# Kernel optimization log

Hardware: AMD Instinct MI355X
Metric: run time of the kernel (lower is better)

## Reference

```python
import jax, jax.numpy as jnp
import numpy as np

EPS = 1e-5

def _offset_conv(x, w, b):
    # 3x3 conv, padding=1, producing 2*K*K offset channels (standard DeformConv2D v1)
    out = jax.lax.conv_general_dilated(x, w, (1, 1), ((1, 1), (1, 1)),
                                       dimension_numbers=('NCHW', 'OIHW', 'NCHW'))
    return out + b[None, :, None, None]

def _bilinear_gather(x, py, px):
    # x: [B,C,H,W]; py,px: [B,K2,H,W] float sample coords -> [B,C,K2,H,W]
    B, C, H, W = x.shape
    py = jnp.clip(py, 0.0, H - 1.0)
    px = jnp.clip(px, 0.0, W - 1.0)
    y0 = jnp.floor(py)
    x0 = jnp.floor(px)
    wy = py - y0
    wx = px - x0
    y0i = y0.astype(jnp.int32)
    x0i = x0.astype(jnp.int32)
    y1i = jnp.minimum(y0i + 1, H - 1)
    x1i = jnp.minimum(x0i + 1, W - 1)
    xf = x.reshape(B, C, H * W)
    K2, Ho, Wo = py.shape[1], py.shape[2], py.shape[3]
    def gather(yy, xx):
        idx = (yy * W + xx).reshape(B, 1, -1)  # broadcast over C
        return jnp.take_along_axis(xf, idx, axis=2).reshape(B, C, K2, Ho, Wo)
    v00 = gather(y0i, x0i)
    v01 = gather(y0i, x1i)
    v10 = gather(y1i, x0i)
    v11 = gather(y1i, x1i)
    wy = wy[:, None]
    wx = wx[:, None]
    return (v00 * (1 - wy) * (1 - wx) + v01 * (1 - wy) * wx
            + v10 * wy * (1 - wx) + v11 * wy * wx)

def _deform_dw(x, w_off, b_off, w_dw, k):
    # depthwise deformable conv, kernel k, padding k//2 (same spatial size)
    B, C, H, W = x.shape
    K2 = k * k
    off = _offset_conv(x, w_off, b_off)      # [B, 2*K2, H, W]
    dy, dx = off[:, :K2], off[:, K2:]
    r = (k - 1) // 2
    pn = jnp.arange(-r, r + 1, dtype=x.dtype)
    pn_y = jnp.repeat(pn, k)[None, :, None, None]  # [1,K2,1,1]
    pn_x = jnp.tile(pn, k)[None, :, None, None]
    gy = jnp.arange(H, dtype=x.dtype)[None, None, :, None]
    gx = jnp.arange(W, dtype=x.dtype)[None, None, None, :]
    py = gy + pn_y + dy
    px = gx + pn_x + dx
    samp = _bilinear_gather(x, py, px)        # [B,C,K2,H,W]
    return jnp.einsum('bckhw,ck->bchw', samp, w_dw.reshape(C, K2))

def _bn_relu(x, g, b, m, v):
    inv = g / jnp.sqrt(v + EPS)
    return jax.nn.relu(x * inv[None, :, None, None] + (b - m * inv)[None, :, None, None])

def setup_inputs() -> dict:
    key = jax.random.key(0)
    B, C, H, W, O = 4, 96, 64, 64, 192
    ks = jax.random.split(key, 32)
    d = {'x': jax.random.normal(ks[0], (B, C, H, W), jnp.float32)}
    i = 1
    for k in (3, 5, 7):
        K2 = k * k
        d[f'w_off{k}'] = 0.01 * jax.random.normal(ks[i], (2 * K2, C, 3, 3), jnp.float32); i += 1
        d[f'b_off{k}'] = jnp.zeros((2 * K2,), jnp.float32)
        d[f'w_dw{k}'] = jax.random.normal(ks[i], (C, k, k), jnp.float32) / k; i += 1
        d[f'g{k}'] = jnp.ones((C,), jnp.float32)
        d[f'be{k}'] = jnp.zeros((C,), jnp.float32)
        d[f'm{k}'] = 0.1 * jax.random.normal(ks[i], (C,), jnp.float32); i += 1
        d[f'v{k}'] = jax.random.uniform(ks[i], (C,), jnp.float32, 0.5, 1.5); i += 1
    d['w_pw'] = jax.random.normal(ks[i], (O, 3 * C), jnp.float32) / np.sqrt(3 * C).astype(np.float32); i += 1
    d['gp'] = jnp.ones((O,), jnp.float32)
    d['bp'] = jnp.zeros((O,), jnp.float32)
    d['mp'] = 0.1 * jax.random.normal(ks[i], (O,), jnp.float32); i += 1
    d['vp'] = jax.random.uniform(ks[i], (O,), jnp.float32, 0.5, 1.5)
    return d

def reference(x, w_off3, b_off3, w_dw3, g3, be3, m3, v3,
              w_off5, b_off5, w_dw5, g5, be5, m5, v5,
              w_off7, b_off7, w_dw7, g7, be7, m7, v7,
              w_pw, gp, bp, mp, vp):
    x1 = _bn_relu(_deform_dw(x, w_off3, b_off3, w_dw3, 3), g3, be3, m3, v3)
    x2 = _bn_relu(_deform_dw(x, w_off5, b_off5, w_dw5, 5), g5, be5, m5, v5)
    x3 = _bn_relu(_deform_dw(x, w_off7, b_off7, w_dw7, 7), g7, be7, m7, v7)
    xc = jnp.concatenate([x1, x2, x3], axis=1)  # [B, 3C, H, W]
    out = jnp.einsum('bchw,oc->bohw', xc, w_pw)  # 1x1 conv
    return _bn_relu(out, gp, bp, mp, vp)
```

## Files before the change

kernel.cpp:

```cpp
#include <hip/hip_runtime.h>
#include <hip/hip_fp16.h>
#include <math.h>

typedef unsigned short u16;
typedef _Float16 f16x8 __attribute__((ext_vector_type(8)));
typedef float f32x4 __attribute__((ext_vector_type(4)));

#define HWp 4096
#define Cc 96
#define Bb 4
#define Oo 192
#define C3 288

#define OFF_WDWT  0
#define OFF_BCAT  14112
#define OFF_SBR   14304
#define OFF_HBR   14592
#define OFF_SPW   14880
#define OFF_HPW   15072
#define FP32_END  15264
#define BF_XTPAD  0
#define BF_WOF    1672704
#define BF_WPW    1838592

__device__ __forceinline__ u16 f2h(float f) { return __half_as_ushort(__float2half(f)); }
__device__ __forceinline__ unsigned h2u(__half2 h) { union { __half2 h; unsigned u; } t; t.h = h; return t.u; }
__device__ __forceinline__ __half2 u2h(unsigned u) { union { __half2 h; unsigned u; } t; t.u = u; return t.h; }

#define PREP_N (165888 + 55296 + 14112 + 192 + 288 + 288 + 192 + 192 + 24960)
#define PREP_BLK ((PREP_N + 255) / 256)

__global__ __launch_bounds__(256) void prep_kernel(
    const float* __restrict__ x,
    const float* __restrict__ w3, const float* __restrict__ b3, const float* __restrict__ dw3,
    const float* __restrict__ g3, const float* __restrict__ be3, const float* __restrict__ m3, const float* __restrict__ v3,
    const float* __restrict__ w5, const float* __restrict__ b5, const float* __restrict__ dw5,
    const float* __restrict__ g5, const float* __restrict__ be5, const float* __restrict__ m5, const float* __restrict__ v5,
    const float* __restrict__ w7, const float* __restrict__ b7, const float* __restrict__ dw7,
    const float* __restrict__ g7, const float* __restrict__ be7, const float* __restrict__ m7, const float* __restrict__ v7,
    const float* __restrict__ wpw,
    const float* __restrict__ gp, const float* __restrict__ bp, const float* __restrict__ mp, const float* __restrict__ vp,
    float* __restrict__ ws)
{
    __shared__ u16 sT[64 * 104];
    u16* bf = (u16*)(ws + FP32_END);
    const int tid = threadIdx.x;

    if (blockIdx.x < 256) {
        const int b = blockIdx.x >> 6, h = blockIdx.x & 63;
        const float* xb = x + (((size_t)b * Cc) << 12) + (h << 6);
#pragma unroll
        for (int it = 0; it < 24; ++it) {
            int j = tid + it * 256;
            int c = j >> 6, p = j & 63;
            sT[p * 104 + c] = f2h(xb[((size_t)c << 12) + p]);
        }
        __syncthreads();
        u16* dst = bf + BF_XTPAD + ((size_t)(b * 66 + h + 1) * 66 + 1) * 96;
#pragma unroll
        for (int it = 0; it < 6; ++it) {
            int j = tid + it * 256;
            int pos = j / 24, c4 = j % 24;
            const u16* s = &sT[pos * 104 + c4 * 4];
            *(uint2*)(dst + pos * 96 + c4 * 4) = make_uint2(
                (unsigned)s[0] | ((unsigned)s[1] << 16),
                (unsigned)s[2] | ((unsigned)s[3] << 16));
        }
        return;
    }

    int i = (blockIdx.x - 256) * 256 + tid;
    if (i < 165888) {
        int f = i / 13824, r = i % 13824;
        int s = r >> 9, l = r & 511;
        int lane = l >> 3, j = l & 7;
        int o = f * 16 + (lane & 15);
        int k = s * 32 + (lane >> 4) * 8 + j;
        int tap = k / 96, c = k % 96;
        float v = 0.f;
        if (o < 18)       v = w3[o * 864 + c * 9 + tap];
        else if (o < 68)  v = w5[(o - 18) * 864 + c * 9 + tap];
        else if (o < 166) v = w7[(o - 68) * 864 + c * 9 + tap];
        bf[BF_WOF + i] = f2h(v);
        return;
    }
    int j = i - 165888;
    if (j < 55296) {
        int f = j / 4608, r = j % 4608;
        int s = r >> 9, l = r & 511;
        int lane = l >> 3, jj = l & 7;
        int o = f * 16 + (lane & 15);
        int k = s * 32 + (lane >> 4) * 8 + jj;
        bf[BF_WPW + j] = f2h(wpw[o * C3 + k]);
        return;
    }
    j -= 55296;
    if (j < 14112) {
        int ksel = j / 4704, rem = j % 4704;
        int t = rem / 96, c = rem % 96;
        int K2 = (ksel == 0) ? 9 : (ksel == 1) ? 25 : 49;
        const float* dw = (ksel == 0) ? dw3 : (ksel == 1) ? dw5 : dw7;
        ws[OFF_WDWT + j] = (t < K2) ? dw[c * K2 + t] : 0.f;
        return;
    }
    j -= 14112;
    if (j < 192) {
        float v = 0.f;
        if (j < 18)       v = b3[j];
        else if (j < 68)  v = b5[j - 18];
        else if (j < 166) v = b7[j - 68];
        ws[OFF_BCAT + j] = v;
        return;
    }
    j -= 192;
    if (j < C3) {
        int ks = j / Cc, c = j % Cc;
        const float* g = (ks == 0) ? g3 : (ks == 1) ? g5 : g7;
        const float* v = (ks == 0) ? v3 : (ks == 1) ? v5 : v7;
        ws[OFF_SBR + j] = g[c] / sqrtf(v[c] + 1e-5f);
        return;
    }
    j -= C3;
    if (j < C3) {
        int ks = j / Cc, c = j % Cc;
        const float* g = (ks == 0) ? g3 : (ks == 1) ? g5 : g7;
        const float* v = (ks == 0) ? v3 : (ks == 1) ? v5 : v7;
        const float* be = (ks == 0) ? be3 : (ks == 1) ? be5 : be7;
        const float* m = (ks == 0) ? m3 : (ks == 1) ? m5 : m7;
        float inv = g[c] / sqrtf(v[c] + 1e-5f);
        ws[OFF_HBR + j] = be[c] - m[c] * inv;
        return;
    }
    j -= C3;
    if (j < Oo) { ws[OFF_SPW + j] = gp[j] / sqrtf(vp[j] + 1e-5f); return; }
    j -= Oo;
    if (j < Oo) {
        float inv = gp[j] / sqrtf(vp[j] + 1e-5f);
        ws[OFF_HPW + j] = bp[j] - mp[j] * inv;
        return;
    }
    j -= Oo;
    if (j < 24960) {
        int c4 = j % 24, rem = j / 24;
        int cell = rem % 260, bb = rem / 260;
        int row, col;
        if (cell < 66)       { row = 0;  col = cell; }
        else if (cell < 132) { row = 65; col = cell - 66; }
        else if (cell < 196) { row = cell - 132 + 1; col = 0; }
        else                 { row = cell - 196 + 1; col = 65; }
        u16* dst = bf + BF_XTPAD + ((size_t)(bb * 66 + row) * 66 + col) * 96 + c4 * 4;
        *(uint2*)dst = make_uint2(0u, 0u);
        return;
    }
}

__global__ __launch_bounds__(256, 4) void mega_kernel(
    const float* __restrict__ ws, float* __restrict__ out)
{
    __shared__ __align__(16) unsigned char shA[15936];
    __shared__ float regB[3072];
    __shared__ float sP1[1728];
    u16* sX = (u16*)shA;
    uint2* sWab = (uint2*)shA;
    unsigned* sPk = (unsigned*)(shA + 10624);
    float* soff = regB;
    u16* ytile = (u16*)regB;

    const u16* bf = (const u16*)(ws + FP32_END);
    const u16* xp = bf + BF_XTPAD;
    const int tid = threadIdx.x;
    const int lane = tid & 63, wid = tid >> 6;
    const int lane15 = lane & 15, quad = lane >> 4;

    const int bx = blockIdx.x;
    const int xcd = bx & 7;
    const int b = xcd >> 1;
    const int tile = ((bx >> 3) << 1) + (xcd & 1);
    const int p0 = tile * 16;
    const int h = p0 >> 6;
    const int w0 = p0 & 63;

    {
        const u16* src = xp + ((size_t)(b * 66 + h) * 66 + w0) * 96;
        for (int j = tid; j < 1296; j += 256) {
            int r = j / 432;
            int rem = j % 432;
            int col = rem / 24, c4 = rem % 24;
            uint2 v = *(const uint2*)(src + ((size_t)(r * 66 + col)) * 96 + c4 * 4);
            *(uint2*)(&sX[(r * 18 + col) * 104 + c4 * 4]) = v;
        }
    }
    __syncthreads();

    {
        const u16* wof = bf + BF_WOF;
        f32x4 acc[3];
#pragma unroll
        for (int ff = 0; ff < 3; ++ff) acc[ff] = (f32x4){0.f, 0.f, 0.f, 0.f};
#pragma unroll
        for (int tap = 0; tap < 9; ++tap) {
            const int ky2 = tap / 3, kx2 = tap % 3;
            const u16* brow = &sX[(ky2 * 18 + kx2 + lane15) * 104 + quad * 8];
#pragma unroll
            for (int cc = 0; cc < 3; ++cc) {
                f16x8 bb = *(const f16x8*)(brow + cc * 32);
                const int s = tap * 3 + cc;
#pragma unroll
                for (int ff = 0; ff < 3; ++ff) {
                    const int f = wid * 3 + ff;
                    f16x8 a = *(const f16x8*)(wof + ((size_t)(f * 27 + s) * 64 + lane) * 8);
                    acc[ff] = __builtin_amdgcn_mfma_f32_16x16x32_f16(a, bb, acc[ff], 0, 0, 0);
                }
            }
        }
        const float* bcat = ws + OFF_BCAT;
#pragma unroll
        for (int ff = 0; ff < 3; ++ff) {
#pragma unroll
            for (int r = 0; r < 4; ++r) {
                int co = (wid * 3 + ff) * 16 + quad * 4 + r;
                soff[co * 16 + lane15] = acc[ff][r] + bcat[co];
            }
        }
    }
    __syncthreads();

    for (int i = tid; i < 1328; i += 256) {
        int gt = i >> 4, q = i & 15;
        int K, K2, R, tb, t;
        if (gt < 9)       { K = 3; K2 = 9;  R = 1; tb = 0;  t = gt; }
        else if (gt < 34) { K = 5; K2 = 25; R = 2; tb = 18; t = gt - 9; }
        else              { K = 7; K2 = 49; R = 3; tb = 68; t = gt - 34; }
        int ky = t / K - R, kx = t % K - R;
        float dy = soff[(tb + t) * 16 + q];
        float dx = soff[(tb + K2 + t) * 16 + q];
        float py = fminf(fmaxf((float)(h + ky) + dy, 0.f), 63.f);
        float px = fminf(fmaxf((float)(w0 + q + kx) + dx, 0.f), 63.f);
        float fy = floorf(py), fx = floorf(px);
        int y0 = (int)fy, x0 = (int)fx;
        float wy = py - fy, wx = px - fx;
        float w11 = wy * wx;
        float w10 = wy - w11;
        float w01 = wx - w11;
        float w00 = 1.f - wy - wx + w11;
        sWab[i] = make_uint2(h2u(__floats2half2_rn(w00, w01)),
                             h2u(__floats2half2_rn(w10, w11)));
        sPk[i] = (unsigned)((y0 + 1) * 66 + (x0 + 1)) * 192u;
    }
    __syncthreads();

#define TAP8(ACC, GT, Q, XCB, WDP) { \
    const uint2 wab = sWab[((GT) << 4) + (Q)]; \
    const unsigned o00 = sPk[((GT) << 4) + (Q)]; \
    const __half2 wAh = u2h(wab.x), wBh = u2h(wab.y); \
    const __half2 w00b = __low2half2(wAh), w01b = __high2half2(wAh); \
    const __half2 w10b = __low2half2(wBh), w11b = __high2half2(wBh); \
    const char* pb = (XCB) + o00; \
    const uint4 u00 = *(const uint4*)(pb); \
    const uint4 u01 = *(const uint4*)(pb + 192); \
    const uint4 u10 = *(const uint4*)(pb + 12672); \
    const uint4 u11 = *(const uint4*)(pb + 12864); \
    const float4 wda = *(const float4*)(WDP); \
    const float4 wdb = *(const float4*)((WDP) + 4); \
    const unsigned a00[4] = {u00.x, u00.y, u00.z, u00.w}; \
    const unsigned a01[4] = {u01.x, u01.y, u01.z, u01.w}; \
    const unsigned a10[4] = {u10.x, u10.y, u10.z, u10.w}; \
    const unsigned a11[4] = {u11.x, u11.y, u11.z, u11.w}; \
    const float wd8[8] = {wda.x, wda.y, wda.z, wda.w, wdb.x, wdb.y, wdb.z, wdb.w}; \
    _Pragma("unroll") \
    for (int d = 0; d < 4; ++d) { \
        __half2 v = __hmul2(w00b, u2h(a00[d])); \
        v = __hfma2(w01b, u2h(a01[d]), v); \
        v = __hfma2(w10b, u2h(a10[d]), v); \
        v = __hfma2(w11b, u2h(a11[d]), v); \
        ACC[2 * d]     = fmaf(wd8[2 * d],     __low2float(v),  ACC[2 * d]); \
        ACC[2 * d + 1] = fmaf(wd8[2 * d + 1], __high2float(v), ACC[2 * d + 1]); \
    } }

#define BN_STORE(ACC, CB, Q) { \
    const float4 sa = *(const float4*)(ws + OFF_SBR + (CB)); \
    const float4 sb = *(const float4*)(ws + OFF_SBR + (CB) + 4); \
    const float4 ha = *(const float4*)(ws + OFF_HBR + (CB)); \
    const float4 hb = *(const float4*)(ws + OFF_HBR + (CB) + 4); \
    const float ss8[8] = {sa.x, sa.y, sa.z, sa.w, sb.x, sb.y, sb.z, sb.w}; \
    const float hh8[8] = {ha.x, ha.y, ha.z, ha.w, hb.x, hb.y, hb.z, hb.w}; \
    unsigned rr[4]; \
    _Pragma("unroll") \
    for (int d = 0; d < 4; ++d) { \
        float lo = fmaxf(fmaf(ACC[2 * d],     ss8[2 * d],     hh8[2 * d]),     0.f); \
        float hi = fmaxf(fmaf(ACC[2 * d + 1], ss8[2 * d + 1], hh8[2 * d + 1]), 0.f); \
        rr[d] = h2u(__floats2half2_rn(lo, hi)); \
    } \
    *(uint4*)(ytile + (Q) * 296 + (CB)) = make_uint4(rr[0], rr[1], rr[2], rr[3]); }

    const u16* xh = xp + (size_t)b * 66 * 66 * 96;

    if (tid < 192) {
        const int c8 = tid % 12;
        const int q  = tid / 12;
        const int c = c8 * 8;
        const char* xcb = (const char*)xh + c * 2;

        {
            float acc[8] = {0.f, 0.f, 0.f, 0.f, 0.f, 0.f, 0.f, 0.f};
            const float* wdT = ws + OFF_WDWT + c;
            for (int gt = 0; gt < 9; ++gt)
                TAP8(acc, gt, q, xcb, wdT + gt * 96);
            BN_STORE(acc, c, q);
        }
        {
            float acc[8] = {0.f, 0.f, 0.f, 0.f, 0.f, 0.f, 0.f, 0.f};
            const float* wdT = ws + OFF_WDWT + 9408 + c;
            for (int gt = 34; gt < 83; ++gt)
                TAP8(acc, gt, q, xcb, wdT + (gt - 34) * 96);
            BN_STORE(acc, 192 + c, q);
        }
        __syncthreads();
        {
            float acc[8] = {0.f, 0.f, 0.f, 0.f, 0.f, 0.f, 0.f, 0.f};
            const float* wdT = ws + OFF_WDWT + 4704 + c;
            for (int gt = 9; gt < 17; ++gt)
                TAP8(acc, gt, q, xcb, wdT + (gt - 9) * 96);
#pragma unroll
            for (int jj = 0; jj < 8; ++jj) acc[jj] += sP1[tid * 9 + jj];
            BN_STORE(acc, 96 + c, q);
        }
    } else {
        const int s = tid - 192;
#pragma unroll 1
        for (int k = 0; k < 3; ++k) {
            const int slot = 3 * s + k;
            const int q2 = slot / 12;
            const int c2 = (slot % 12) * 8;
            const char* xcb2 = (const char*)xh + c2 * 2;
            const float* wdT = ws + OFF_WDWT + 4704 + c2;
            float acc[8] = {0.f, 0.f, 0.f, 0.f, 0.f, 0.f, 0.f, 0.f};
            for (int gt = 17; gt < 34; ++gt)
                TAP8(acc, gt, q2, xcb2, wdT + (gt - 9) * 96);
#pragma unroll
            for (int jj = 0; jj < 8; ++jj) sP1[slot * 9 + jj] = acc[jj];
        }
        __syncthreads();
    }
    __syncthreads();

    {
        const u16* wpw = bf + BF_WPW;
        f32x4 acc[3];
#pragma unroll
        for (int ff = 0; ff < 3; ++ff) acc[ff] = (f32x4){0.f, 0.f, 0.f, 0.f};
        const u16* brow = &ytile[lane15 * 296 + quad * 8];
#pragma unroll
        for (int s = 0; s < 9; ++s) {
            f16x8 bb = *(const f16x8*)(brow + s * 32);
#pragma unroll
            for (int ff = 0; ff < 3; ++ff) {
                const int f = wid * 3 + ff;
                f16x8 a = *(const f16x8*)(wpw + ((size_t)(f * 9 + s) * 64 + lane) * 8);
                acc[ff] = __builtin_amdgcn_mfma_f32_16x16x32_f16(a, bb, acc[ff], 0, 0, 0);
            }
        }
        const float* spw = ws + OFF_SPW;
        const float* hpw = ws + OFF_HPW;
        const int p = p0 + lane15;
#pragma unroll
        for (int ff = 0; ff < 3; ++ff) {
#pragma unroll
            for (int r = 0; r < 4; ++r) {
                int o = (wid * 3 + ff) * 16 + quad * 4 + r;
                out[(((size_t)(b * Oo + o)) << 12) + p] =
                    fmaxf(fmaf(acc[ff][r], spw[o], hpw[o]), 0.f);
            }
        }
    }
}

extern "C" void kernel_launch(void* const* d_in, const int* in_sizes, int n_in,
                              void* d_out, int out_size, void* d_ws, size_t ws_size,
                              hipStream_t stream)
{
    const float* x     = (const float*)d_in[0];
    const float* w3    = (const float*)d_in[1];
    const float* b3    = (const float*)d_in[2];
    const float* dw3   = (const float*)d_in[3];
    const float* g3    = (const float*)d_in[4];
    const float* be3   = (const float*)d_in[5];
    const float* m3    = (const float*)d_in[6];
    const float* v3    = (const float*)d_in[7];
    const float* w5    = (const float*)d_in[8];
    const float* b5    = (const float*)d_in[9];
    const float* dw5   = (const float*)d_in[10];
    const float* g5    = (const float*)d_in[11];
    const float* be5   = (const float*)d_in[12];
    const float* m5    = (const float*)d_in[13];
    const float* v5    = (const float*)d_in[14];
    const float* w7    = (const float*)d_in[15];
    const float* b7    = (const float*)d_in[16];
    const float* dw7   = (const float*)d_in[17];
    const float* g7    = (const float*)d_in[18];
    const float* be7   = (const float*)d_in[19];
    const float* m7    = (const float*)d_in[20];
    const float* v7    = (const float*)d_in[21];
    const float* wpw   = (const float*)d_in[22];
    const float* gp    = (const float*)d_in[23];
    const float* bp    = (const float*)d_in[24];
    const float* mp    = (const float*)d_in[25];
    const float* vp    = (const float*)d_in[26];

    float* ws = (float*)d_ws;
    float* out = (float*)d_out;

    {
        prep_kernel<<<256 + PREP_BLK, 256, 0, stream>>>(
            x,
            w3, b3, dw3, g3, be3, m3, v3,
            w5, b5, dw5, g5, be5, m5, v5,
            w7, b7, dw7, g7, be7, m7, v7,
            wpw, gp, bp, mp, vp, ws);
    }
    {
        mega_kernel<<<1024, 256, 0, stream>>>(ws, out);
    }
}
```

Baseline: 178.7 us.

## Stage input rows in a shared-memory ring buffer for bilinear gathers

Bilinear samples for the three deformable depthwise convs now come from a 3-row LDS ring buffer holding a 27-pixel-wide window of the padded input. The buffer is refilled row by row as the kernel-row loop advances, and samples that fall outside the window fall back to global loads. Taps are reorganized by kernel row so all three kernel sizes accumulate together. This replaces the old split of 192 compute threads plus 64 helper threads and drops the sP1 partial-sum buffer. Per-sample metadata shrinks to packed half (wy,wx) and a 16-bit coordinate, with the four bilinear weights recomputed in half precision. The cost is extra barriers per row, divergent branches, and idle threads 192-255 during the gather phase.

```diff
diff --git a/kernel.cpp b/kernel.cpp
--- a/kernel.cpp
+++ b/kernel.cpp
@@ -154,15 +154,18 @@
     }
 }
 
+#define RING_COLS 27
+#define RING_PSTR 208
+#define RING_SLOT (RING_COLS * RING_PSTR)
 __global__ __launch_bounds__(256, 4) void mega_kernel(
     const float* __restrict__ ws, float* __restrict__ out)
 {
-    __shared__ __align__(16) unsigned char shA[15936];
+    __shared__ __align__(16) unsigned char shA[11232];
     __shared__ float regB[3072];
-    __shared__ float sP1[1728];
+    __shared__ __align__(16) unsigned char ring[3 * RING_SLOT];
     u16* sX = (u16*)shA;
-    uint2* sWab = (uint2*)shA;
-    unsigned* sPk = (unsigned*)(shA + 10624);
+    unsigned* sWxy = (unsigned*)shA;
+    u16* sPk2 = (u16*)(shA + 5312);
     float* soff = regB;
     u16* ytile = (u16*)regB;
 
@@ -179,6 +182,9 @@
     const int p0 = tile * 16;
     const int h = p0 >> 6;
     const int w0 = p0 & 63;
+    const int cb0 = w0 - 4;
+
+    const char* xbb = (const char*)(xp + (size_t)b * 66 * 66 * 96);
 
     {
         const u16* src = xp + ((size_t)(b * 66 + h) * 66 + w0) * 96;
@@ -188,6 +194,18 @@
             int col = rem / 24, c4 = rem % 24;
             uint2 v = *(const uint2*)(src + ((size_t)(r * 66 + col)) * 96 + c4 * 4);
             *(uint2*)(&sX[(r * 18 + col) * 104 + c4 * 4]) = v;
+        }
+    }
+    {
+#pragma unroll
+        for (int r = 0; r < 3; ++r) {
+            const int rp = h - 3 + r;
+            const int base = (rp * 66 + cb0) * 192;
+            const int sl = ((rp + 3) % 3) * RING_SLOT;
+            for (int j = tid; j < 324; j += 256) {
+                *(uint4*)(ring + sl + (j / 12) * RING_PSTR + (j % 12) * 16) =
+                    *(const uint4*)(xbb + base + (j / 12) * 192 + (j % 12) * 16);
+            }
         }
     }
     __syncthreads();
@@ -239,27 +257,38 @@
         float fy = floorf(py), fx = floorf(px);
         int y0 = (int)fy, x0 = (int)fx;
         float wy = py - fy, wx = px - fx;
-        float w11 = wy * wx;
-        float w10 = wy - w11;
-        float w01 = wx - w11;
-        float w00 = 1.f - wy - wx + w11;
-        sWab[i] = make_uint2(h2u(__floats2half2_rn(w00, w01)),
-                             h2u(__floats2half2_rn(w10, w11)));
-        sPk[i] = (unsigned)((y0 + 1) * 66 + (x0 + 1)) * 192u;
+        sWxy[i] = h2u(__floats2half2_rn(wy, wx));
+        sPk2[i] = (u16)((y0 + 1) | ((x0 + 1) << 7));
     }
     __syncthreads();
 
-#define TAP8(ACC, GT, Q, XCB, WDP) { \
-    const uint2 wab = sWab[((GT) << 4) + (Q)]; \
-    const unsigned o00 = sPk[((GT) << 4) + (Q)]; \
-    const __half2 wAh = u2h(wab.x), wBh = u2h(wab.y); \
-    const __half2 w00b = __low2half2(wAh), w01b = __high2half2(wAh); \
-    const __half2 w10b = __low2half2(wBh), w11b = __high2half2(wBh); \
-    const char* pb = (XCB) + o00; \
-    const uint4 u00 = *(const uint4*)(pb); \
-    const uint4 u01 = *(const uint4*)(pb + 192); \
-    const uint4 u10 = *(const uint4*)(pb + 12672); \
-    const uint4 u11 = *(const uint4*)(pb + 12864); \
+#define TAPL(ACC, GT, WDP) { \
+    const unsigned pk = sPk2[((GT) << 4) + q]; \
+    const unsigned wxy = sWxy[((GT) << 4) + q]; \
+    const int y0p = (int)(pk & 127u), x0p = (int)(pk >> 7); \
+    const int rel = y0p - rowp; \
+    const int cl  = x0p - cb0; \
+    uint4 u00, u01, u10, u11; \
+    if (((unsigned)rel <= 1u) && ((unsigned)cl <= 25u)) { \
+        int s0 = bs + rel; s0 = (s0 >= 3) ? s0 - 3 : s0; \
+        int s1 = s0 + 1;   s1 = (s1 >= 3) ? s1 - 3 : s1; \
+        const unsigned char* p0 = ring + s0 * RING_SLOT + cl * RING_PSTR + c8off; \
+        const unsigned char* p1 = ring + s1 * RING_SLOT + cl * RING_PSTR + c8off; \
+        u00 = *(const uint4*)(p0); u01 = *(const uint4*)(p0 + RING_PSTR); \
+        u10 = *(const uint4*)(p1); u11 = *(const uint4*)(p1 + RING_PSTR); \
+    } else { \
+        const char* pb = xbb + (y0p * 66 + x0p) * 192 + c8off; \
+        u00 = *(const uint4*)(pb); u01 = *(const uint4*)(pb + 192); \
+        u10 = *(const uint4*)(pb + 12672); u11 = *(const uint4*)(pb + 12864); \
+    } \
+    const __half2 wyx = u2h(wxy); \
+    const __half wyh = __low2half(wyx), wxh = __high2half(wyx); \
+    const __half h11 = __hmul(wyh, wxh); \
+    const __half h10 = __hsub(wyh, h11); \
+    const __half h01 = __hsub(wxh, h11); \
+    const __half h00 = __hsub(__hsub(__ushort_as_half((unsigned short)0x3C00), wyh), h01); \
+    const __half2 w00b = __half2half2(h00), w01b = __half2half2(h01); \
+    const __half2 w10b = __half2half2(h10), w11b = __half2half2(h11); \
     const float4 wda = *(const float4*)(WDP); \
     const float4 wdb = *(const float4*)((WDP) + 4); \
     const unsigned a00[4] = {u00.x, u00.y, u00.z, u00.w}; \
@@ -293,54 +322,72 @@
     } \
     *(uint4*)(ytile + (Q) * 296 + (CB)) = make_uint4(rr[0], rr[1], rr[2], rr[3]); }
 
-    const u16* xh = xp + (size_t)b * 66 * 66 * 96;
-
-    if (tid < 192) {
+    {
         const int c8 = tid % 12;
         const int q  = tid / 12;
-        const int c = c8 * 8;
-        const char* xcb = (const char*)xh + c * 2;
-
-        {
-            float acc[8] = {0.f, 0.f, 0.f, 0.f, 0.f, 0.f, 0.f, 0.f};
-            const float* wdT = ws + OFF_WDWT + c;
-            for (int gt = 0; gt < 9; ++gt)
-                TAP8(acc, gt, q, xcb, wdT + gt * 96);
-            BN_STORE(acc, c, q);
-        }
-        {
-            float acc[8] = {0.f, 0.f, 0.f, 0.f, 0.f, 0.f, 0.f, 0.f};
-            const float* wdT = ws + OFF_WDWT + 9408 + c;
-            for (int gt = 34; gt < 83; ++gt)
-                TAP8(acc, gt, q, xcb, wdT + (gt - 34) * 96);
-            BN_STORE(acc, 192 + c, q);
-        }
-        __syncthreads();
-        {
-            float acc[8] = {0.f, 0.f, 0.f, 0.f, 0.f, 0.f, 0.f, 0.f};
-            const float* wdT = ws + OFF_WDWT + 4704 + c;
-            for (int gt = 9; gt < 17; ++gt)
-                TAP8(acc, gt, q, xcb, wdT + (gt - 9) * 96);
-#pragma unroll
-            for (int jj = 0; jj < 8; ++jj) acc[jj] += sP1[tid * 9 + jj];
-            BN_STORE(acc, 96 + c, q);
-        }
-    } else {
-        const int s = tid - 192;
+        const int c8off = c8 * 16;
+        const float* wd0 = ws + OFF_WDWT + c8 * 8;
+        const float* wd1 = ws + OFF_WDWT + 4704 + c8 * 8;
+        const float* wd2 = ws + OFF_WDWT + 9408 + c8 * 8;
+        float accA[8] = {0.f, 0.f, 0.f, 0.f, 0.f, 0.f, 0.f, 0.f};
+        float accB[8] = {0.f, 0.f, 0.f, 0.f, 0.f, 0.f, 0.f, 0.f};
+        float accC[8] = {0.f, 0.f, 0.f, 0.f, 0.f, 0.f, 0.f, 0.f};
+
 #pragma unroll 1
-        for (int k = 0; k < 3; ++k) {
-            const int slot = 3 * s + k;
-            const int q2 = slot / 12;
-            const int c2 = (slot % 12) * 8;
-            const char* xcb2 = (const char*)xh + c2 * 2;
-            const float* wdT = ws + OFF_WDWT + 4704 + c2;
-            float acc[8] = {0.f, 0.f, 0.f, 0.f, 0.f, 0.f, 0.f, 0.f};
-            for (int gt = 17; gt < 34; ++gt)
-                TAP8(acc, gt, q2, xcb2, wdT + (gt - 9) * 96);
-#pragma unroll
-            for (int jj = 0; jj < 8; ++jj) sP1[slot * 9 + jj] = acc[jj];
-        }
-        __syncthreads();
+        for (int kyi = 0; kyi < 7; ++kyi) {
+            const int ky = kyi - 3;
+            const int rowp = h + ky;
+            const int bs = (h + kyi) % 3;
+
+            uint4 st0, st1;
+            if (kyi < 6) {
+                const int base = ((h + kyi) * 66 + cb0) * 192;
+                st0 = *(const uint4*)(xbb + base + (tid / 12) * 192 + (tid % 12) * 16);
+                if (tid < 68) {
+                    const int j2 = tid + 256;
+                    st1 = *(const uint4*)(xbb + base + (j2 / 12) * 192 + (j2 % 12) * 16);
+                }
+            }
+
+            if (tid < 192) {
+                if (ky >= -1 && ky <= 1) {
+                    const int t0 = (ky + 1) * 3;
+#pragma unroll
+                    for (int j = 0; j < 3; ++j)
+                        TAPL(accA, t0 + j, wd0 + (t0 + j) * 96);
+                }
+                if (ky >= -2 && ky <= 2) {
+                    const int t1 = (ky + 2) * 5;
+#pragma unroll
+                    for (int j = 0; j < 5; ++j)
+                        TAPL(accB, 9 + t1 + j, wd1 + (t1 + j) * 96);
+                }
+                {
+                    const int t2 = (ky + 3) * 7;
+#pragma unroll
+                    for (int j = 0; j < 7; ++j)
+                        TAPL(accC, 34 + t2 + j, wd2 + (t2 + j) * 96);
+                }
+            }
+
+            if (kyi < 6) {
+                __syncthreads();
+                const int sl = bs * RING_SLOT;
+                *(uint4*)(ring + sl + (tid / 12) * RING_PSTR + (tid % 12) * 16) = st0;
+                if (tid < 68) {
+                    const int j2 = tid + 256;
+                    *(uint4*)(ring + sl + (j2 / 12) * RING_PSTR + (j2 % 12) * 16) = st1;
+                }
+                __syncthreads();
+            }
+        }
+
+        if (tid < 192) {
+            const int c = c8 * 8;
+            BN_STORE(accA, c, q);
+            BN_STORE(accB, 96 + c, q);
+            BN_STORE(accC, 192 + c, q);
+        }
     }
     __syncthreads();
 
```

After: 444.0 us. 149% more time.

## Stage 9x24 input window in LDS and gather bilinear taps from shared memory

Applied to the files above, without the earlier changes.

Loads a 9-row by 24-column halo window of the padded input (all 96 channels) into LDS per block. Bilinear sample corners that fall inside the window are read from LDS, and the rest fall back to global memory through a packed flag index. Bilinear weights are now stored as (wy, wx) in fp16 and the four corner weights are recomputed in the tap loop. The earlier work split, where threads 192 to 255 computed part of the 5x5 branch, is removed, so only 192 threads do the gather. The larger LDS footprint drops launch bounds to 2 blocks per SM, which trades occupancy for fewer global gathers.

```diff
diff --git a/kernel.cpp b/kernel.cpp
--- a/kernel.cpp
+++ b/kernel.cpp
@@ -154,15 +154,15 @@
     }
 }
 
-__global__ __launch_bounds__(256, 4) void mega_kernel(
+#define WIN_PSTR 208
+#define WIN_RSTR (24 * WIN_PSTR)
+__global__ __launch_bounds__(256, 2) void mega_kernel(
     const float* __restrict__ ws, float* __restrict__ out)
 {
-    __shared__ __align__(16) unsigned char shA[15936];
+    __shared__ __align__(16) unsigned char win[9 * WIN_RSTR];
+    __shared__ unsigned sWxy[1328];
+    __shared__ u16 sPk[1328];
     __shared__ float regB[3072];
-    __shared__ float sP1[1728];
-    u16* sX = (u16*)shA;
-    uint2* sWab = (uint2*)shA;
-    unsigned* sPk = (unsigned*)(shA + 10624);
     float* soff = regB;
     u16* ytile = (u16*)regB;
 
@@ -180,15 +180,15 @@
     const int h = p0 >> 6;
     const int w0 = p0 & 63;
 
-    {
-        const u16* src = xp + ((size_t)(b * 66 + h) * 66 + w0) * 96;
-        for (int j = tid; j < 1296; j += 256) {
-            int r = j / 432;
-            int rem = j % 432;
-            int col = rem / 24, c4 = rem % 24;
-            uint2 v = *(const uint2*)(src + ((size_t)(r * 66 + col)) * 96 + c4 * 4);
-            *(uint2*)(&sX[(r * 18 + col) * 104 + c4 * 4]) = v;
-        }
+    const char* xbb = (const char*)(xp + (size_t)b * 66 * 66 * 96);
+
+    for (int j = tid; j < 2592; j += 256) {
+        int cell = j / 12, k = j - cell * 12;
+        int r = cell / 24, c = cell - r * 24;
+        int rr = h - 3 + r; rr = rr < 0 ? 0 : (rr > 65 ? 65 : rr);
+        int cc = w0 - 3 + c; cc = cc < 0 ? 0 : (cc > 65 ? 65 : cc);
+        *(uint4*)(win + cell * WIN_PSTR + k * 16) =
+            *(const uint4*)(xbb + (rr * 66 + cc) * 192 + k * 16);
     }
     __syncthreads();
 
@@ -200,7 +200,8 @@
 #pragma unroll
         for (int tap = 0; tap < 9; ++tap) {
             const int ky2 = tap / 3, kx2 = tap % 3;
-            const u16* brow = &sX[(ky2 * 18 + kx2 + lane15) * 104 + quad * 8];
+            const u16* brow = (const u16*)win +
+                ((size_t)((3 + ky2) * 24 + 3 + kx2 + lane15)) * 104 + quad * 8;
 #pragma unroll
             for (int cc = 0; cc < 3; ++cc) {
                 f16x8 bb = *(const f16x8*)(brow + cc * 32);
@@ -239,27 +240,42 @@
         float fy = floorf(py), fx = floorf(px);
         int y0 = (int)fy, x0 = (int)fx;
         float wy = py - fy, wx = px - fx;
-        float w11 = wy * wx;
-        float w10 = wy - w11;
-        float w01 = wx - w11;
-        float w00 = 1.f - wy - wx + w11;
-        sWab[i] = make_uint2(h2u(__floats2half2_rn(w00, w01)),
-                             h2u(__floats2half2_rn(w10, w11)));
-        sPk[i] = (unsigned)((y0 + 1) * 66 + (x0 + 1)) * 192u;
+        int y0p = y0 + 1, x0p = x0 + 1;
+        int slot = y0p - h + 3;
+        int cell = x0p - w0 + 3;
+        unsigned pk;
+        if ((unsigned)slot <= 7u && (unsigned)cell <= 22u)
+            pk = (unsigned)((slot * 24 + cell) * 13);
+        else
+            pk = 0x8000u | ((unsigned)y0p << 7) | (unsigned)x0p;
+        sWxy[i] = h2u(__floats2half2_rn(wy, wx));
+        sPk[i] = (u16)pk;
     }
     __syncthreads();
 
-#define TAP8(ACC, GT, Q, XCB, WDP) { \
-    const uint2 wab = sWab[((GT) << 4) + (Q)]; \
-    const unsigned o00 = sPk[((GT) << 4) + (Q)]; \
-    const __half2 wAh = u2h(wab.x), wBh = u2h(wab.y); \
-    const __half2 w00b = __low2half2(wAh), w01b = __high2half2(wAh); \
-    const __half2 w10b = __low2half2(wBh), w11b = __high2half2(wBh); \
-    const char* pb = (XCB) + o00; \
-    const uint4 u00 = *(const uint4*)(pb); \
-    const uint4 u01 = *(const uint4*)(pb + 192); \
-    const uint4 u10 = *(const uint4*)(pb + 12672); \
-    const uint4 u11 = *(const uint4*)(pb + 12864); \
+#define TAPW(ACC, GT, WDP) { \
+    const unsigned pk = sPk[((GT) << 4) + q]; \
+    const unsigned wxy = sWxy[((GT) << 4) + q]; \
+    uint4 u00, u01, u10, u11; \
+    if (!(pk & 0x8000u)) { \
+        const unsigned char* wb = win + pk * 16 + c8off; \
+        u00 = *(const uint4*)(wb); \
+        u01 = *(const uint4*)(wb + WIN_PSTR); \
+        u10 = *(const uint4*)(wb + WIN_RSTR); \
+        u11 = *(const uint4*)(wb + WIN_RSTR + WIN_PSTR); \
+    } else { \
+        const char* pb = xbb + (((int)((pk >> 7) & 127u)) * 66 + (int)(pk & 127u)) * 192 + c8off; \
+        u00 = *(const uint4*)(pb);         u01 = *(const uint4*)(pb + 192); \
+        u10 = *(const uint4*)(pb + 12672); u11 = *(const uint4*)(pb + 12864); \
+    } \
+    const __half2 wyx = u2h(wxy); \
+    const __half wyh = __low2half(wyx), wxh = __high2half(wyx); \
+    const __half h11 = __hmul(wyh, wxh); \
+    const __half h10 = __hsub(wyh, h11); \
+    const __half h01 = __hsub(wxh, h11); \
+    const __half h00 = __hsub(__hsub(__ushort_as_half((unsigned short)0x3C00), wyh), h01); \
+    const __half2 w00b = __half2half2(h00), w01b = __half2half2(h01); \
+    const __half2 w10b = __half2half2(h10), w11b = __half2half2(h11); \
     const float4 wda = *(const float4*)(WDP); \
     const float4 wdb = *(const float4*)((WDP) + 4); \
     const unsigned a00[4] = {u00.x, u00.y, u00.z, u00.w}; \
@@ -293,54 +309,33 @@
     } \
     *(uint4*)(ytile + (Q) * 296 + (CB)) = make_uint4(rr[0], rr[1], rr[2], rr[3]); }
 
-    const u16* xh = xp + (size_t)b * 66 * 66 * 96;
-
     if (tid < 192) {
         const int c8 = tid % 12;
         const int q  = tid / 12;
         const int c = c8 * 8;
-        const char* xcb = (const char*)xh + c * 2;
+        const int c8off = c8 * 16;
 
         {
             float acc[8] = {0.f, 0.f, 0.f, 0.f, 0.f, 0.f, 0.f, 0.f};
             const float* wdT = ws + OFF_WDWT + c;
             for (int gt = 0; gt < 9; ++gt)
-                TAP8(acc, gt, q, xcb, wdT + gt * 96);
+                TAPW(acc, gt, wdT + gt * 96);
             BN_STORE(acc, c, q);
+        }
+        {
+            float acc[8] = {0.f, 0.f, 0.f, 0.f, 0.f, 0.f, 0.f, 0.f};
+            const float* wdT = ws + OFF_WDWT + 4704 + c;
+            for (int gt = 9; gt < 34; ++gt)
+                TAPW(acc, gt, wdT + (gt - 9) * 96);
+            BN_STORE(acc, 96 + c, q);
         }
         {
             float acc[8] = {0.f, 0.f, 0.f, 0.f, 0.f, 0.f, 0.f, 0.f};
             const float* wdT = ws + OFF_WDWT + 9408 + c;
             for (int gt = 34; gt < 83; ++gt)
-                TAP8(acc, gt, q, xcb, wdT + (gt - 34) * 96);
+                TAPW(acc, gt, wdT + (gt - 34) * 96);
             BN_STORE(acc, 192 + c, q);
         }
-        __syncthreads();
-        {
-            float acc[8] = {0.f, 0.f, 0.f, 0.f, 0.f, 0.f, 0.f, 0.f};
-            const float* wdT = ws + OFF_WDWT + 4704 + c;
-            for (int gt = 9; gt < 17; ++gt)
-                TAP8(acc, gt, q, xcb, wdT + (gt - 9) * 96);
-#pragma unroll
-            for (int jj = 0; jj < 8; ++jj) acc[jj] += sP1[tid * 9 + jj];
-            BN_STORE(acc, 96 + c, q);
-        }
-    } else {
-        const int s = tid - 192;
-#pragma unroll 1
-        for (int k = 0; k < 3; ++k) {
-            const int slot = 3 * s + k;
-            const int q2 = slot / 12;
-            const int c2 = (slot % 12) * 8;
-            const char* xcb2 = (const char*)xh + c2 * 2;
-            const float* wdT = ws + OFF_WDWT + 4704 + c2;
-            float acc[8] = {0.f, 0.f, 0.f, 0.f, 0.f, 0.f, 0.f, 0.f};
-            for (int gt = 17; gt < 34; ++gt)
-                TAP8(acc, gt, q2, xcb2, wdT + (gt - 9) * 96);
-#pragma unroll
-            for (int jj = 0; jj < 8; ++jj) sP1[slot * 9 + jj] = acc[jj];
-        }
-        __syncthreads();
     }
     __syncthreads();
 
```

Result: slower. 217.6 us (+21.8%).

## Drop 4th-wave split of 5x5 taps and pack sample weights with offsets

Applied to the files above, without the earlier changes.

Removes the scheme where the fourth wavefront computed part of the 5x5 deformable taps into a shared partial buffer that the first three waves added in after an extra barrier. The first three waves now do all 5x5 taps themselves. Bilinear weights and gather offsets are packed into one 16-byte shared entry, so each tap needs a single LDS load instead of two. This removes the intra-block barrier and the partial-sum buffer, but leaves wave 3 idle during the gather phase and lengthens the critical path of waves 0-2.

```diff
diff --git a/kernel.cpp b/kernel.cpp
--- a/kernel.cpp
+++ b/kernel.cpp
@@ -157,12 +157,10 @@
 __global__ __launch_bounds__(256, 4) void mega_kernel(
     const float* __restrict__ ws, float* __restrict__ out)
 {
-    __shared__ __align__(16) unsigned char shA[15936];
+    __shared__ __align__(16) unsigned char shA[21248];
     __shared__ float regB[3072];
-    __shared__ float sP1[1728];
     u16* sX = (u16*)shA;
-    uint2* sWab = (uint2*)shA;
-    unsigned* sPk = (unsigned*)(shA + 10624);
+    uint4* sWI = (uint4*)shA;
     float* soff = regB;
     u16* ytile = (u16*)regB;
 
@@ -243,19 +241,19 @@
         float w10 = wy - w11;
         float w01 = wx - w11;
         float w00 = 1.f - wy - wx + w11;
-        sWab[i] = make_uint2(h2u(__floats2half2_rn(w00, w01)),
-                             h2u(__floats2half2_rn(w10, w11)));
-        sPk[i] = (unsigned)((y0 + 1) * 66 + (x0 + 1)) * 192u;
+        unsigned wA = h2u(__floats2half2_rn(w00, w01));
+        unsigned wB = h2u(__floats2half2_rn(w10, w11));
+        unsigned o00 = (unsigned)((y0 + 1) * 66 + (x0 + 1)) * 192u;
+        sWI[i] = make_uint4(wA, wB, o00, 0u);
     }
     __syncthreads();
 
 #define TAP8(ACC, GT, Q, XCB, WDP) { \
-    const uint2 wab = sWab[((GT) << 4) + (Q)]; \
-    const unsigned o00 = sPk[((GT) << 4) + (Q)]; \
-    const __half2 wAh = u2h(wab.x), wBh = u2h(wab.y); \
+    const uint4 e = sWI[((GT) << 4) + (Q)]; \
+    const __half2 wAh = u2h(e.x), wBh = u2h(e.y); \
     const __half2 w00b = __low2half2(wAh), w01b = __high2half2(wAh); \
     const __half2 w10b = __low2half2(wBh), w11b = __high2half2(wBh); \
-    const char* pb = (XCB) + o00; \
+    const char* pb = (XCB) + e.z; \
     const uint4 u00 = *(const uint4*)(pb); \
     const uint4 u01 = *(const uint4*)(pb + 192); \
     const uint4 u10 = *(const uint4*)(pb + 12672); \
@@ -293,12 +291,11 @@
     } \
     *(uint4*)(ytile + (Q) * 296 + (CB)) = make_uint4(rr[0], rr[1], rr[2], rr[3]); }
 
-    const u16* xh = xp + (size_t)b * 66 * 66 * 96;
-
     if (tid < 192) {
         const int c8 = tid % 12;
         const int q  = tid / 12;
         const int c = c8 * 8;
+        const u16* xh = xp + (size_t)b * 66 * 66 * 96;
         const char* xcb = (const char*)xh + c * 2;
 
         {
@@ -310,37 +307,18 @@
         }
         {
             float acc[8] = {0.f, 0.f, 0.f, 0.f, 0.f, 0.f, 0.f, 0.f};
+            const float* wdT = ws + OFF_WDWT + 4704 + c;
+            for (int gt = 9; gt < 34; ++gt)
+                TAP8(acc, gt, q, xcb, wdT + (gt - 9) * 96);
+            BN_STORE(acc, 96 + c, q);
+        }
+        {
+            float acc[8] = {0.f, 0.f, 0.f, 0.f, 0.f, 0.f, 0.f, 0.f};
             const float* wdT = ws + OFF_WDWT + 9408 + c;
             for (int gt = 34; gt < 83; ++gt)
                 TAP8(acc, gt, q, xcb, wdT + (gt - 34) * 96);
             BN_STORE(acc, 192 + c, q);
         }
-        __syncthreads();
-        {
-            float acc[8] = {0.f, 0.f, 0.f, 0.f, 0.f, 0.f, 0.f, 0.f};
-            const float* wdT = ws + OFF_WDWT + 4704 + c;
-            for (int gt = 9; gt < 17; ++gt)
-                TAP8(acc, gt, q, xcb, wdT + (gt - 9) * 96);
-#pragma unroll
-            for (int jj = 0; jj < 8; ++jj) acc[jj] += sP1[tid * 9 + jj];
-            BN_STORE(acc, 96 + c, q);
-        }
-    } else {
-        const int s = tid - 192;
-#pragma unroll 1
-        for (int k = 0; k < 3; ++k) {
-            const int slot = 3 * s + k;
-            const int q2 = slot / 12;
-            const int c2 = (slot % 12) * 8;
-            const char* xcb2 = (const char*)xh + c2 * 2;
-            const float* wdT = ws + OFF_WDWT + 4704 + c2;
-            float acc[8] = {0.f, 0.f, 0.f, 0.f, 0.f, 0.f, 0.f, 0.f};
-            for (int gt = 17; gt < 34; ++gt)
-                TAP8(acc, gt, q2, xcb2, wdT + (gt - 9) * 96);
-#pragma unroll
-            for (int jj = 0; jj < 8; ++jj) sP1[slot * 9 + jj] = acc[jj];
-        }
-        __syncthreads();
     }
     __syncthreads();
 
```

Result: no change. 177.7 us (-0.5%).
